# Performance work log

Hardware: AMD Instinct MI355X
Metric: run time of the kernel (lower is better)

The kernel has to match this reference:

```python
import jax, jax.numpy as jnp
import numpy as np

S, M, V, E, H = 128, 256, 32000, 1024, 512
PAD_ID = V - 1  # pad_id=-1 normalized to vocab-1


def setup_inputs() -> dict:
    key = jax.random.key(0)
    ks = jax.random.split(key, 9)
    F_lens = jax.random.randint(ks[0], (M,), 1, S + 1)
    tok = jax.random.randint(ks[1], (S, M), 1, PAD_ID)  # avoid 0 and PAD for valid tokens
    valid = jnp.arange(S)[:, None] < F_lens[None, :]
    F = jnp.where(valid, tok, PAD_ID)
    sc = 1.0 / np.sqrt(H)
    emb = jax.random.normal(ks[2], (V, E), jnp.float32) * 0.02
    emb = emb.at[PAD_ID].set(0.0)
    # PyTorch LSTM layout: gates [i, f, g, o]; bias_ih + bias_hh folded into one b.
    Wih0 = jax.random.uniform(ks[3], (2, 4 * H, E), jnp.float32, -sc, sc)
    Whh0 = jax.random.uniform(ks[4], (2, 4 * H, H), jnp.float32, -sc, sc)
    b0 = jax.random.uniform(ks[5], (2, 4 * H), jnp.float32, -sc, sc)
    Wih1 = jax.random.uniform(ks[6], (2, 4 * H, 2 * H), jnp.float32, -sc, sc)
    Whh1 = jax.random.uniform(ks[7], (2, 4 * H, H), jnp.float32, -sc, sc)
    b1 = jax.random.uniform(ks[8], (2, 4 * H), jnp.float32, -sc, sc)
    return dict(F=F, F_lens=F_lens, emb=emb, Wih0=Wih0, Whh0=Whh0, b0=b0,
                Wih1=Wih1, Whh1=Whh1, b1=b1)


def _run_lstm(x, mask, Wih, Whh, b):
    # x: [S, M, D], mask: [S, M] bool (update state only where valid, as packed seq does)
    m_ = x.shape[1]
    h_dim = Whh.shape[1]

    def step(carry, inp):
        h, c = carry
        xt, mt = inp
        g = xt @ Wih.T + h @ Whh.T + b
        i, f, gg, o = jnp.split(g, 4, axis=-1)
        c2 = jax.nn.sigmoid(f) * c + jax.nn.sigmoid(i) * jnp.tanh(gg)
        h2 = jax.nn.sigmoid(o) * jnp.tanh(c2)
        mt = mt[:, None]
        h2 = jnp.where(mt, h2, h)
        c2 = jnp.where(mt, c2, c)
        return (h2, c2), h2

    init = (jnp.zeros((m_, h_dim), x.dtype), jnp.zeros((m_, h_dim), x.dtype))
    _, hs = jax.lax.scan(step, init, (x, mask))
    return hs


def _bilstm_layer(x, mask, idx, Wih, Whh, b):
    # forward direction
    hf = _run_lstm(x, mask, Wih[0], Whh[0], b[0])
    # backward direction: per-sequence reverse within valid length (packed semantics)
    xr = jnp.take_along_axis(x, idx[:, :, None], axis=0)
    hb = _run_lstm(xr, mask, Wih[1], Whh[1], b[1])
    hb = jnp.take_along_axis(hb, idx[:, :, None], axis=0)  # idx is an involution on valid t
    return jnp.concatenate([hf, hb], axis=-1)


def reference(F, F_lens, emb, Wih0, Whh0, b0, Wih1, Whh1, b1):
    s_ = F.shape[0]
    t = jnp.arange(s_)[:, None]
    valid = t < F_lens[None, :]                      # [S, M]
    idx = jnp.where(valid, F_lens[None, :] - 1 - t, t)
    # embedding with padding_idx zeroing (matches nn.Embedding padding_idx + explicit loop)
    x = jnp.where((F != PAD_ID)[:, :, None], emb[F], 0.0)
    h1 = _bilstm_layer(x, valid, idx, Wih0, Whh0, b0)
    h2 = _bilstm_layer(h1, valid, idx, Wih1, Whh1, b1)
    # pad_packed_sequence(padding_value=h_pad=0) + final F==0 masking loop, fused
    keep = valid & (F != 0)
    return jnp.where(keep[:, :, None], h2, 0.0)
```

## Files before the change

kernel.cpp:

```cpp
#include <hip/hip_runtime.h>
#include <hip/hip_bf16.h>

#define S_LEN 128
#define M_B   256
#define E_DIM 1024
#define H_DIM 512
#define G4    2048
#define N_ROWS (S_LEN*M_B)
#define KD    1024

typedef __bf16 bf16_t;
typedef __bf16 bf16x8 __attribute__((ext_vector_type(8)));
typedef float  f32x4  __attribute__((ext_vector_type(4)));
typedef int    i32x4  __attribute__((ext_vector_type(4)));

#define AS1(p) ((const __attribute__((address_space(1))) void*)(p))
#define AS3(p) ((__attribute__((address_space(3))) void*)(p))

__device__ __forceinline__ float sigm(float x)     { return 1.f / (1.f + __expf(-x)); }
__device__ __forceinline__ float tanhfast(float x) { return 2.f / (1.f + __expf(-2.f * x)) - 1.f; }

__device__ __forceinline__ void store_h_dev(bf16_t* p, bf16_t v) {
    unsigned int w = (unsigned int)__builtin_bit_cast(unsigned short, v);
    asm volatile("global_store_short %0, %1, off sc0 sc1" :: "v"(p), "v"(w) : "memory");
}
__device__ __forceinline__ bf16x8 load_h_dev(const bf16_t* p) {
    i32x4 r;
    asm volatile("global_load_dwordx4 %0, %1, off sc0 sc1" : "=v"(r) : "v"(p) : "memory");
    return __builtin_bit_cast(bf16x8, r);
}
__device__ __forceinline__ f32x4 load_pv4(const float* p) {
    f32x4 r;
    asm volatile("global_load_dwordx4 %0, %1, off" : "=v"(r) : "v"(p) : "memory");
    return r;
}
__device__ __forceinline__ void store_flag(unsigned int* p, unsigned int v) {
    asm volatile("global_store_dword %0, %1, off sc0 sc1" :: "v"(p), "v"(v) : "memory");
}
__device__ __forceinline__ unsigned int load_flag(const unsigned int* p) {
    unsigned int r;
    asm volatile("global_load_dword %0, %1, off sc0 sc1\n\ts_waitcnt vmcnt(0)"
                 : "=v"(r) : "v"(p) : "memory");
    return r;
}

__global__ __launch_bounds__(256)
void permute_all_kernel(const float* __restrict__ Wih0, const float* __restrict__ Whh0,
                        const float* __restrict__ b0,
                        const float* __restrict__ Wih1, const float* __restrict__ Whh1,
                        const float* __restrict__ b1,
                        bf16_t* __restrict__ Wih0p, bf16_t* __restrict__ Whh0p,
                        bf16_t* __restrict__ Wih1p, bf16_t* __restrict__ Whh1p,
                        float* __restrict__ b0p, float* __restrict__ b1p)
{
    int bid = blockIdx.x;
    int lay = bid >> 12;
    int d   = (bid >> 11) & 1;
    int jp  = bid & 2047;
    int q = jp >> 6, r = jp & 63;
    int gate = r >> 4, u16 = r & 15;
    int j = gate * H_DIM + q * 16 + u16;

    const float* Wih = lay ? Wih1 : Wih0;
    const float* Whh = lay ? Whh1 : Whh0;
    const float* b   = lay ? b1 : b0;
    bf16_t* Wihp = lay ? Wih1p : Wih0p;
    bf16_t* Whhp = lay ? Whh1p : Whh0p;
    float*  bp   = lay ? b1p : b0p;

    const float* s_ih = Wih + ((size_t)d * G4 + j) * E_DIM;
    bf16_t*      d_ih = Wihp + ((size_t)d * G4 + jp) * E_DIM;
    for (int e = threadIdx.x; e < E_DIM; e += 256) d_ih[e] = (bf16_t)s_ih[e];

    const float* s_hh = Whh + ((size_t)d * G4 + j) * H_DIM;
    bf16_t*      d_hh = Whhp + ((size_t)d * G4 + jp) * H_DIM;
    for (int k = threadIdx.x; k < H_DIM; k += 256) d_hh[k] = (bf16_t)s_hh[k];

    if (threadIdx.x == 0) bp[d * G4 + jp] = b[d * G4 + j];
}

__global__ __launch_bounds__(256)
void embed_kernel(const int* __restrict__ F, const float* __restrict__ emb,
                  const int* __restrict__ F_lens,
                  bf16_t* __restrict__ X, int* __restrict__ srcrow)
{
    int n   = blockIdx.x;
    int tok = F[n];
    const float4* src = (const float4*)(emb + (size_t)tok * E_DIM);
    bf16_t*       dst = X + (size_t)n * E_DIM;
    for (int i = threadIdx.x; i < E_DIM / 4; i += 256) {
        float4 v = src[i];
        dst[i * 4 + 0] = (bf16_t)v.x;
        dst[i * 4 + 1] = (bf16_t)v.y;
        dst[i * 4 + 2] = (bf16_t)v.z;
        dst[i * 4 + 3] = (bf16_t)v.w;
    }
    if (threadIdx.x == 0) {
        int t = n >> 8, m = n & 255;
        int L = F_lens[m];
        int st = (t < L) ? (L - 1 - t) : t;
        srcrow[n] = st * M_B + m;
    }
}

#define BM 128
#define BN 128
#define BKG 64

__global__ __launch_bounds__(256)
void gemm_pre_kernel(const bf16_t* __restrict__ A,
                     const bf16_t* __restrict__ Wp,
                     const float* __restrict__ bp,
                     const int* __restrict__ srcrow,
                     float* __restrict__ PREc,
                     int rowbase, int TCR)
{
    const int nwg = gridDim.x;
    const int qx  = nwg >> 3;
    const int orig = blockIdx.x;
    const int wg   = (orig & 7) * qx + (orig >> 3);
    const int MT   = TCR / BM;
    const int n_t  = wg & 15;
    const int m_t  = (wg >> 4) % MT;
    const int d    = wg / (16 * MT);

    const int n0   = n_t * BN;
    const int mloc = m_t * BM;
    const int tid  = threadIdx.x;
    const int lane = tid & 63, wave = tid >> 6;
    const int wm = wave >> 1, wn = wave & 1;
    const int fr = lane & 15, fq = lane >> 4;

    __shared__ __attribute__((aligned(16))) bf16_t At[BM * BKG];
    __shared__ __attribute__((aligned(16))) bf16_t Bt[BN * BKG];

    const int rA = tid >> 3;
    const int co = (((tid & 7) ^ (rA & 7)) << 3);
    size_t srowA[4];
    const bf16_t* Bp[4];
#pragma unroll
    for (int it = 0; it < 4; ++it) {
        int nn = rowbase + mloc + rA + it * 32;
        srowA[it] = (d == 1) ? (size_t)srcrow[nn] : (size_t)nn;
        Bp[it] = Wp + ((size_t)d * G4 + n0 + rA + it * 32) * KD + co;
    }

    f32x4 acc[4][4];
#pragma unroll
    for (int i = 0; i < 4; ++i)
#pragma unroll
        for (int j = 0; j < 4; ++j) { f32x4 z = {0.f, 0.f, 0.f, 0.f}; acc[i][j] = z; }

    for (int kt = 0; kt < KD; kt += BKG) {
#pragma unroll
        for (int it = 0; it < 4; ++it)
            __builtin_amdgcn_global_load_lds(AS1(A + srowA[it] * KD + kt + co),
                                             AS3(&At[(it * 256 + wave * 64) * 8]), 16, 0, 0);
#pragma unroll
        for (int it = 0; it < 4; ++it)
            __builtin_amdgcn_global_load_lds(AS1(Bp[it] + kt),
                                             AS3(&Bt[(it * 256 + wave * 64) * 8]), 16, 0, 0);
        __syncthreads();

        bf16x8 af[2][4], bff[2][4];
#pragma unroll
        for (int ks = 0; ks < 2; ++ks) {
#pragma unroll
            for (int i = 0; i < 4; ++i) {
                int ra = wm * 64 + i * 16 + fr;
                int ca = (ks * 4 + fq) ^ (ra & 7);
                af[ks][i] = *(const bf16x8*)&At[ra * BKG + ca * 8];
                int rb = wn * 64 + i * 16 + fr;
                int cbk = (ks * 4 + fq) ^ (rb & 7);
                bff[ks][i] = *(const bf16x8*)&Bt[rb * BKG + cbk * 8];
            }
        }
#pragma unroll
        for (int ks = 0; ks < 2; ++ks)
#pragma unroll
            for (int i = 0; i < 4; ++i)
#pragma unroll
                for (int j = 0; j < 4; ++j)
                    acc[i][j] = __builtin_amdgcn_mfma_f32_16x16x32_bf16(af[ks][i], bff[ks][j], acc[i][j], 0, 0, 0);
        __syncthreads();
    }

    const int ucol = ((n0 >> 6) + wn) * 16 + fr;
    float bq[4];
#pragma unroll
    for (int g = 0; g < 4; ++g) bq[g] = bp[d * G4 + n0 + wn * 64 + fr + g * 16];
#pragma unroll
    for (int mi = 0; mi < 4; ++mi) {
#pragma unroll
        for (int rr = 0; rr < 4; ++rr) {
            int r = mloc + wm * 64 + mi * 16 + fq * 4 + rr;
            f32x4 v;
#pragma unroll
            for (int g = 0; g < 4; ++g) v[g] = acc[mi][g][rr] + bq[g];
            *(f32x4*)&PREc[(((size_t)d * TCR + r) * 512 + ucol) * 4] = v;
        }
    }
}

__global__ __launch_bounds__(256)
void lstm_chunk_kernel(const bf16_t* __restrict__ Whhp,
                       const float* __restrict__ PREc,
                       const int* __restrict__ F_lens,
                       float* __restrict__ cfb,
                       bf16_t* __restrict__ hbA,
                       bf16_t* __restrict__ hbB,
                       bf16_t* __restrict__ H1,
                       float* __restrict__ OUT,
                       unsigned int* __restrict__ flags,
                       int t0, int TC, int TCR, int mode, int s_base)
{
    const int d  = blockIdx.z;
    const int bx = blockIdx.x;
    const int m0 = blockIdx.y * 64;
    const int tid = threadIdx.x;
    const int lane = tid & 63, wave = tid >> 6;
    const int fr = lane & 15, fq = lane >> 4;
    unsigned int* gflags = flags + (((blockIdx.y << 1) | d) << 5);

    __shared__ __attribute__((aligned(16))) bf16_t Bt[64 * 512];
    __shared__ unsigned int arr[4];
    __shared__ unsigned int go_w;

    const bf16_t* Bg = Whhp + ((size_t)d * G4 + bx * 64) * H_DIM;
#pragma unroll
    for (int it = 0; it < 16; ++it) {
        int c   = it * 256 + tid;
        int row = c >> 6, ck = c & 63;
        int cks = ck ^ (row & 7);
        __builtin_amdgcn_global_load_lds(AS1(Bg + (size_t)row * H_DIM + cks * 8),
                                         AS3(&Bt[(it * 256 + wave * 64) * 8]), 16, 0, 0);
    }

    if (tid < 4) __hip_atomic_store(&arr[tid], (unsigned int)s_base,
                                    __ATOMIC_RELAXED, __HIP_MEMORY_SCOPE_WORKGROUP);
    if (tid == 0) __hip_atomic_store(&go_w, (unsigned int)s_base,
                                     __ATOMIC_RELAXED, __HIP_MEMORY_SCOPE_WORKGROUP);

    const int mrow  = m0 + wave * 16 + fr;
    const int u     = bx * 16 + fr;
    int mm[4], LL[4], sidx[4];
    float c_own[4], h_own[4];
    const float* pbase[4];
#pragma unroll
    for (int rr = 0; rr < 4; ++rr) {
        mm[rr]   = m0 + wave * 16 + fq * 4 + rr;
        LL[rr]   = F_lens[mm[rr]];
        sidx[rr] = (d * M_B + mm[rr]) * H_DIM + u;
        c_own[rr]= cfb[sidx[rr]];
        pbase[rr]= PREc + (((size_t)d * TCR + mm[rr]) * 512 + u) * 4;
    }
    {
        const bf16_t* hin0 = (t0 & 1) ? hbB : hbA;
#pragma unroll
        for (int rr = 0; rr < 4; ++rr) h_own[rr] = (float)hin0[sidx[rr]];
    }

    f32x4 pv[4];
#pragma unroll
    for (int rr = 0; rr < 4; ++rr)
        pv[rr] = load_pv4(pbase[rr]);

    __syncthreads();

    for (int tt = 0; tt < TC; ++tt) {
        const int t = t0 + tt;
        const unsigned int tgt = (unsigned int)(s_base + tt + 1);
        const bf16_t* hin  = (t & 1) ? hbB : hbA;
        bf16_t*       hout = (t & 1) ? hbA : hbB;

        const bf16_t* Arow = hin + ((size_t)d * M_B + mrow) * H_DIM + fq * 8;
        bf16x8 af[16];
#pragma unroll
        for (int ks = 0; ks < 16; ++ks)
            af[ks] = load_h_dev(Arow + ks * 32);
        asm volatile("s_waitcnt vmcnt(0)" ::: "memory");
        __builtin_amdgcn_sched_barrier(0);

        f32x4 acc[4];
#pragma unroll
        for (int j = 0; j < 4; ++j) { f32x4 z = {0.f, 0.f, 0.f, 0.f}; acc[j] = z; }

#pragma unroll
        for (int ks = 0; ks < 16; ++ks) {
#pragma unroll
            for (int j = 0; j < 4; ++j) {
                int rb = j * 16 + fr;
                int ck = (ks * 4 + fq) ^ (rb & 7);
                bf16x8 bf = *(const bf16x8*)&Bt[rb * 512 + ck * 8];
                acc[j] = __builtin_amdgcn_mfma_f32_16x16x32_bf16(af[ks], bf, acc[j], 0, 0, 0);
            }
        }

#pragma unroll
        for (int rr = 0; rr < 4; ++rr) {
            bool mt = (t < LL[rr]);
            float gi = acc[0][rr] + pv[rr][0];
            float gf = acc[1][rr] + pv[rr][1];
            float gg = acc[2][rr] + pv[rr][2];
            float go = acc[3][rr] + pv[rr][3];
            float c2 = sigm(gf) * c_own[rr] + sigm(gi) * tanhfast(gg);
            float h2 = sigm(go) * tanhfast(c2);
            if (!mt) { c2 = c_own[rr]; h2 = h_own[rr]; }
            c_own[rr] = c2;
            h_own[rr] = h2;
            store_h_dev(&hout[sidx[rr]], (bf16_t)h2);
        }
        asm volatile("s_waitcnt vmcnt(0)" ::: "memory");
        if (lane == 0)
            __hip_atomic_store(&arr[wave], tgt, __ATOMIC_RELAXED, __HIP_MEMORY_SCOPE_WORKGROUP);

#pragma unroll
        for (int rr = 0; rr < 4; ++rr) {
            bool mt = (t < LL[rr]);
            int trow = (d == 0 || !mt) ? t : (LL[rr] - 1 - t);
            size_t orow = (size_t)trow * M_B + mm[rr];
            if (mode == 0) H1[orow * 1024 + d * H_DIM + u] = (bf16_t)h_own[rr];
            else           OUT[orow * 1024 + d * H_DIM + u] = mt ? h_own[rr] : 0.f;
        }
        f32x4 pvn[4];
        if (tt + 1 < TC) {
#pragma unroll
            for (int rr = 0; rr < 4; ++rr)
                pvn[rr] = load_pv4(pbase[rr] + (size_t)(tt + 1) * ((size_t)M_B * G4));
        }

        if (wave == 0) {
            for (;;) {
                unsigned int a0 = __hip_atomic_load(&arr[0], __ATOMIC_RELAXED, __HIP_MEMORY_SCOPE_WORKGROUP);
                unsigned int a1 = __hip_atomic_load(&arr[1], __ATOMIC_RELAXED, __HIP_MEMORY_SCOPE_WORKGROUP);
                unsigned int a2 = __hip_atomic_load(&arr[2], __ATOMIC_RELAXED, __HIP_MEMORY_SCOPE_WORKGROUP);
                unsigned int a3 = __hip_atomic_load(&arr[3], __ATOMIC_RELAXED, __HIP_MEMORY_SCOPE_WORKGROUP);
                unsigned int mn = min(min(a0, a1), min(a2, a3));
                if (mn >= tgt) break;
                __builtin_amdgcn_s_sleep(1);
            }
            if (lane == 0) store_flag(&gflags[bx], tgt);
            const unsigned int* fp = &gflags[lane & 31];
            while (__ballot(load_flag(fp) >= tgt) != ~0ull)
                __builtin_amdgcn_s_sleep(1);
            if (lane == 0)
                __hip_atomic_store(&go_w, tgt, __ATOMIC_RELAXED, __HIP_MEMORY_SCOPE_WORKGROUP);
        } else {
            while (__hip_atomic_load(&go_w, __ATOMIC_RELAXED, __HIP_MEMORY_SCOPE_WORKGROUP) < tgt)
                __builtin_amdgcn_s_sleep(1);
        }

        if (tt + 1 < TC) {
#pragma unroll
            for (int rr = 0; rr < 4; ++rr)
                pv[rr] = pvn[rr];
        }
    }

#pragma unroll
    for (int rr = 0; rr < 4; ++rr) cfb[sidx[rr]] = c_own[rr];
}

extern "C" void kernel_launch(void* const* d_in, const int* in_sizes, int n_in,
                              void* d_out, int out_size, void* d_ws, size_t ws_size,
                              hipStream_t stream)
{
    const int*   F      = (const int*)d_in[0];
    const int*   F_lens = (const int*)d_in[1];
    const float* emb    = (const float*)d_in[2];
    const float* Wih0   = (const float*)d_in[3];
    const float* Whh0   = (const float*)d_in[4];
    const float* b0     = (const float*)d_in[5];
    const float* Wih1   = (const float*)d_in[6];
    const float* Whh1   = (const float*)d_in[7];
    const float* b1     = (const float*)d_in[8];
    float* OUT = (float*)d_out;

    char* p = (char*)d_ws;
    auto alloc = [&](size_t bytes) { char* q = p; p += (bytes + 255) & ~(size_t)255; return (void*)q; };
    bf16_t* X0    = (bf16_t*)alloc((size_t)N_ROWS * E_DIM * 2);
    bf16_t* H1    = (bf16_t*)alloc((size_t)N_ROWS * 1024 * 2);
    bf16_t* Wih0p = (bf16_t*)alloc((size_t)2 * G4 * E_DIM * 2);
    bf16_t* Whh0p = (bf16_t*)alloc((size_t)2 * G4 * H_DIM * 2);
    bf16_t* Wih1p = (bf16_t*)alloc((size_t)2 * G4 * E_DIM * 2);
    bf16_t* Whh1p = (bf16_t*)alloc((size_t)2 * G4 * H_DIM * 2);
    float*  b0p   = (float*)alloc((size_t)2 * G4 * 4);
    float*  b1p   = (float*)alloc((size_t)2 * G4 * 4);
    int*    srcrow= (int*)alloc((size_t)N_ROWS * 4);
    bf16_t* hbA   = (bf16_t*)alloc((size_t)2 * M_B * H_DIM * 2);
    bf16_t* hbB   = (bf16_t*)alloc((size_t)2 * M_B * H_DIM * 2);
    float*  cfb   = (float*)alloc((size_t)2 * M_B * H_DIM * 4);
    unsigned int* flags = (unsigned int*)alloc(4096);
    size_t base_used = (size_t)(p - (char*)d_ws);

    int TC = 0;
    const int tcs[8] = {128, 64, 32, 16, 8, 4, 2, 1};
    for (int i = 0; i < 8; ++i) {
        size_t need = base_used + (size_t)2 * tcs[i] * M_B * G4 * 4;
        if (need <= ws_size) { TC = tcs[i]; break; }
    }
    if (TC == 0) return;
    float* PREc = (float*)p;
    const int TCR = TC * M_B;

    hipMemsetAsync(flags, 0, 4096, stream);
    permute_all_kernel<<<dim3(2 * 2 * G4), 256, 0, stream>>>(
        Wih0, Whh0, b0, Wih1, Whh1, b1, Wih0p, Whh0p, Wih1p, Whh1p, b0p, b1p);
    embed_kernel<<<dim3(N_ROWS), 256, 0, stream>>>(F, emb, F_lens, X0, srcrow);

    for (int layer = 0; layer < 2; ++layer) {
        const bf16_t* Xin  = layer ? H1 : X0;
        const bf16_t* Wihp = layer ? Wih1p : Wih0p;
        const bf16_t* Whhp = layer ? Whh1p : Whh0p;
        const float*  bp   = layer ? b1p : b0p;

        hipMemsetAsync(hbA, 0, (size_t)2 * M_B * H_DIM * 2, stream);
        hipMemsetAsync(cfb, 0, (size_t)2 * M_B * H_DIM * 4, stream);

        for (int c = 0; c < S_LEN / TC; ++c) {
            gemm_pre_kernel<<<dim3(2 * (TCR / BM) * 16), 256, 0, stream>>>(
                Xin, Wihp, bp, srcrow, PREc, c * TCR, TCR);

            lstm_chunk_kernel<<<dim3(32, 4, 2), dim3(256), 0, stream>>>(
                Whhp, PREc, F_lens, cfb, hbA, hbB, H1, OUT, flags,
                c * TC, TC, TCR, layer, layer * S_LEN + c * TC);
        }
    }
}
```

Baseline: 2.320 ms.

## Halve recurrent LSTM grid by giving each block 32 hidden units

Each recurrent block now covers 128 permuted gate rows (32 hidden units), so it keeps twice as much of Whh in LDS (128 KB) and runs two accumulator groups per wave. The grid drops from 32 to 16 blocks along x, which halves the number of blocks in each per-step cross-block flag barrier and halves redundant loads of the h state per step. In exchange each block does twice the MFMA and gate work per timestep, and the larger LDS footprint and register use may reduce occupancy.

```diff
diff --git a/kernel.cpp b/kernel.cpp
--- a/kernel.cpp
+++ b/kernel.cpp
@@ -222,13 +222,13 @@
     const int fr = lane & 15, fq = lane >> 4;
     unsigned int* gflags = flags + (((blockIdx.y << 1) | d) << 5);
 
-    __shared__ __attribute__((aligned(16))) bf16_t Bt[64 * 512];
+    __shared__ __attribute__((aligned(16))) bf16_t Bt[128 * 512];
     __shared__ unsigned int arr[4];
     __shared__ unsigned int go_w;
 
-    const bf16_t* Bg = Whhp + ((size_t)d * G4 + bx * 64) * H_DIM;
-#pragma unroll
-    for (int it = 0; it < 16; ++it) {
+    const bf16_t* Bg = Whhp + ((size_t)d * G4 + bx * 128) * H_DIM;
+#pragma unroll
+    for (int it = 0; it < 32; ++it) {
         int c   = it * 256 + tid;
         int row = c >> 6, ck = c & 63;
         int cks = ck ^ (row & 7);
@@ -242,28 +242,36 @@
                                      __ATOMIC_RELAXED, __HIP_MEMORY_SCOPE_WORKGROUP);
 
     const int mrow  = m0 + wave * 16 + fr;
-    const int u     = bx * 16 + fr;
-    int mm[4], LL[4], sidx[4];
-    float c_own[4], h_own[4];
+    int mm[4], LL[4];
+    int sidx[2][4];
+    float c_own[2][4], h_own[2][4];
     const float* pbase[4];
 #pragma unroll
     for (int rr = 0; rr < 4; ++rr) {
-        mm[rr]   = m0 + wave * 16 + fq * 4 + rr;
-        LL[rr]   = F_lens[mm[rr]];
-        sidx[rr] = (d * M_B + mm[rr]) * H_DIM + u;
-        c_own[rr]= cfb[sidx[rr]];
-        pbase[rr]= PREc + (((size_t)d * TCR + mm[rr]) * 512 + u) * 4;
+        mm[rr] = m0 + wave * 16 + fq * 4 + rr;
+        LL[rr] = F_lens[mm[rr]];
+        pbase[rr] = PREc + (((size_t)d * TCR + mm[rr]) * 512 + bx * 32 + fr) * 4;
+#pragma unroll
+        for (int qg = 0; qg < 2; ++qg)
+            sidx[qg][rr] = (d * M_B + mm[rr]) * H_DIM + bx * 32 + qg * 16 + fr;
     }
     {
         const bf16_t* hin0 = (t0 & 1) ? hbB : hbA;
 #pragma unroll
-        for (int rr = 0; rr < 4; ++rr) h_own[rr] = (float)hin0[sidx[rr]];
-    }
-
-    f32x4 pv[4];
-#pragma unroll
-    for (int rr = 0; rr < 4; ++rr)
-        pv[rr] = load_pv4(pbase[rr]);
+        for (int qg = 0; qg < 2; ++qg)
+#pragma unroll
+            for (int rr = 0; rr < 4; ++rr) {
+                c_own[qg][rr] = cfb[sidx[qg][rr]];
+                h_own[qg][rr] = (float)hin0[sidx[qg][rr]];
+            }
+    }
+
+    f32x4 pv[2][4];
+#pragma unroll
+    for (int qg = 0; qg < 2; ++qg)
+#pragma unroll
+        for (int rr = 0; rr < 4; ++rr)
+            pv[qg][rr] = load_pv4(pbase[rr] + qg * 64);
 
     __syncthreads();
 
@@ -281,35 +289,41 @@
         asm volatile("s_waitcnt vmcnt(0)" ::: "memory");
         __builtin_amdgcn_sched_barrier(0);
 
-        f32x4 acc[4];
-#pragma unroll
-        for (int j = 0; j < 4; ++j) { f32x4 z = {0.f, 0.f, 0.f, 0.f}; acc[j] = z; }
+        f32x4 acc[2][4];
+#pragma unroll
+        for (int qg = 0; qg < 2; ++qg)
+#pragma unroll
+            for (int j = 0; j < 4; ++j) { f32x4 z = {0.f, 0.f, 0.f, 0.f}; acc[qg][j] = z; }
 
 #pragma unroll
         for (int ks = 0; ks < 16; ++ks) {
 #pragma unroll
-            for (int j = 0; j < 4; ++j) {
-                int rb = j * 16 + fr;
-                int ck = (ks * 4 + fq) ^ (rb & 7);
-                bf16x8 bf = *(const bf16x8*)&Bt[rb * 512 + ck * 8];
-                acc[j] = __builtin_amdgcn_mfma_f32_16x16x32_bf16(af[ks], bf, acc[j], 0, 0, 0);
+            for (int qg = 0; qg < 2; ++qg)
+#pragma unroll
+                for (int j = 0; j < 4; ++j) {
+                    int rb = qg * 64 + j * 16 + fr;
+                    int ck = (ks * 4 + fq) ^ (rb & 7);
+                    bf16x8 bf = *(const bf16x8*)&Bt[rb * 512 + ck * 8];
+                    acc[qg][j] = __builtin_amdgcn_mfma_f32_16x16x32_bf16(af[ks], bf, acc[qg][j], 0, 0, 0);
+                }
+        }
+
+#pragma unroll
+        for (int qg = 0; qg < 2; ++qg)
+#pragma unroll
+            for (int rr = 0; rr < 4; ++rr) {
+                bool mt = (t < LL[rr]);
+                float gi = acc[qg][0][rr] + pv[qg][rr][0];
+                float gf = acc[qg][1][rr] + pv[qg][rr][1];
+                float gg = acc[qg][2][rr] + pv[qg][rr][2];
+                float go = acc[qg][3][rr] + pv[qg][rr][3];
+                float c2 = sigm(gf) * c_own[qg][rr] + sigm(gi) * tanhfast(gg);
+                float h2 = sigm(go) * tanhfast(c2);
+                if (!mt) { c2 = c_own[qg][rr]; h2 = h_own[qg][rr]; }
+                c_own[qg][rr] = c2;
+                h_own[qg][rr] = h2;
+                store_h_dev(&hout[sidx[qg][rr]], (bf16_t)h2);
             }
-        }
-
-#pragma unroll
-        for (int rr = 0; rr < 4; ++rr) {
-            bool mt = (t < LL[rr]);
-            float gi = acc[0][rr] + pv[rr][0];
-            float gf = acc[1][rr] + pv[rr][1];
-            float gg = acc[2][rr] + pv[rr][2];
-            float go = acc[3][rr] + pv[rr][3];
-            float c2 = sigm(gf) * c_own[rr] + sigm(gi) * tanhfast(gg);
-            float h2 = sigm(go) * tanhfast(c2);
-            if (!mt) { c2 = c_own[rr]; h2 = h_own[rr]; }
-            c_own[rr] = c2;
-            h_own[rr] = h2;
-            store_h_dev(&hout[sidx[rr]], (bf16_t)h2);
-        }
         asm volatile("s_waitcnt vmcnt(0)" ::: "memory");
         if (lane == 0)
             __hip_atomic_store(&arr[wave], tgt, __ATOMIC_RELAXED, __HIP_MEMORY_SCOPE_WORKGROUP);
@@ -319,14 +333,19 @@
             bool mt = (t < LL[rr]);
             int trow = (d == 0 || !mt) ? t : (LL[rr] - 1 - t);
             size_t orow = (size_t)trow * M_B + mm[rr];
-            if (mode == 0) H1[orow * 1024 + d * H_DIM + u] = (bf16_t)h_own[rr];
-            else           OUT[orow * 1024 + d * H_DIM + u] = mt ? h_own[rr] : 0.f;
-        }
-        f32x4 pvn[4];
+#pragma unroll
+            for (int qg = 0; qg < 2; ++qg) {
+                int u = bx * 32 + qg * 16 + fr;
+                if (mode == 0) H1[orow * 1024 + d * H_DIM + u] = (bf16_t)h_own[qg][rr];
+                else           OUT[orow * 1024 + d * H_DIM + u] = mt ? h_own[qg][rr] : 0.f;
+            }
+        }
         if (tt + 1 < TC) {
 #pragma unroll
-            for (int rr = 0; rr < 4; ++rr)
-                pvn[rr] = load_pv4(pbase[rr] + (size_t)(tt + 1) * ((size_t)M_B * G4));
+            for (int qg = 0; qg < 2; ++qg)
+#pragma unroll
+                for (int rr = 0; rr < 4; ++rr)
+                    pv[qg][rr] = load_pv4(pbase[rr] + (size_t)(tt + 1) * ((size_t)M_B * G4) + qg * 64);
         }
 
         if (wave == 0) {
@@ -340,7 +359,7 @@
                 __builtin_amdgcn_s_sleep(1);
             }
             if (lane == 0) store_flag(&gflags[bx], tgt);
-            const unsigned int* fp = &gflags[lane & 31];
+            const unsigned int* fp = &gflags[lane & 15];
             while (__ballot(load_flag(fp) >= tgt) != ~0ull)
                 __builtin_amdgcn_s_sleep(1);
             if (lane == 0)
@@ -349,16 +368,13 @@
             while (__hip_atomic_load(&go_w, __ATOMIC_RELAXED, __HIP_MEMORY_SCOPE_WORKGROUP) < tgt)
                 __builtin_amdgcn_s_sleep(1);
         }
-
-        if (tt + 1 < TC) {
-#pragma unroll
-            for (int rr = 0; rr < 4; ++rr)
-                pv[rr] = pvn[rr];
-        }
-    }
-
-#pragma unroll
-    for (int rr = 0; rr < 4; ++rr) cfb[sidx[rr]] = c_own[rr];
+    }
+
+#pragma unroll
+    for (int qg = 0; qg < 2; ++qg)
+#pragma unroll
+        for (int rr = 0; rr < 4; ++rr)
+            cfb[sidx[qg][rr]] = c_own[qg][rr];
 }
 
 extern "C" void kernel_launch(void* const* d_in, const int* in_sizes, int n_in,
@@ -421,7 +437,7 @@
             gemm_pre_kernel<<<dim3(2 * (TCR / BM) * 16), 256, 0, stream>>>(
                 Xin, Wihp, bp, srcrow, PREc, c * TCR, TCR);
 
-            lstm_chunk_kernel<<<dim3(32, 4, 2), dim3(256), 0, stream>>>(
+            lstm_chunk_kernel<<<dim3(16, 4, 2), dim3(256), 0, stream>>>(
                 Whhp, PREc, F_lens, cfb, hbA, hbB, H1, OUT, flags,
                 c * TC, TC, TCR, layer, layer * S_LEN + c * TC);
         }
```

After: 3.008 ms. 1.3x slower.
